# Kernel tuning notes

Hardware: AMD Instinct MI355X
Metric: run time of the kernel (lower is better)

## Reference

```python
import jax, jax.numpy as jnp
import numpy as np

B, C, H, W = 8, 128, 64, 64
HEADS = 8
HID = 512  # dim * ffn_expansion_factor


def conv1x1(x, w):
    # x: (b,c,h,w), w: (o,c)
    return jnp.einsum('bchw,oc->bohw', x, w)


def dwconv(x, w):
    # depthwise conv, w: (c,1,k,k), same padding
    k = w.shape[-1]
    p = k // 2
    return jax.lax.conv_general_dilated(
        x, w, window_strides=(1, 1), padding=((p, p), (p, p)),
        dimension_numbers=('NCHW', 'OIHW', 'NCHW'),
        feature_group_count=x.shape[1])


def ln_channels(x, w, b):
    # WithBias LayerNorm over channel dim (torch does it on b,(hw),c layout)
    mu = x.mean(axis=1, keepdims=True)
    var = x.var(axis=1, keepdims=True)
    return (x - mu) / jnp.sqrt(var + 1e-5) * w[None, :, None, None] + b[None, :, None, None]


def l2norm(x):
    # torch F.normalize along last dim, eps=1e-12
    n = jnp.linalg.norm(x, axis=-1, keepdims=True)
    return x / jnp.maximum(n, 1e-12)


def setup_inputs() -> dict:
    key = jax.random.key(0)
    ks = list(jax.random.split(key, 24))
    it = iter(ks)

    def nrm(shape, s=0.05):
        return (jax.random.normal(next(it), shape, jnp.float32) * s)

    d = {}
    d['x'] = jax.random.normal(next(it), (B, C, H, W), jnp.float32)
    d['ln1_w'] = jnp.ones((C,), jnp.float32)
    d['ln1_b'] = jnp.zeros((C,), jnp.float32)
    d['temp'] = jnp.ones((HEADS, 1, 1), jnp.float32)
    d['wq'] = nrm((C, C))
    d['wk'] = nrm((C, C))
    d['wv'] = nrm((C, C))
    for k in (3, 5, 7):
        for n in ('q', 'k', 'v'):
            d['dw%s%d' % (n, k)] = nrm((C, 1, k, k))
    d['attn_po'] = nrm((C, 3 * C))
    d['ln2_w'] = jnp.ones((C,), jnp.float32)
    d['ln2_b'] = jnp.zeros((C,), jnp.float32)
    d['ffn_in'] = nrm((2 * HID, C))
    for k in (3, 5, 7):
        d['ffn_dw%d' % k] = nrm((2 * HID, 1, k, k))
    d['ffn_po'] = nrm((C, 3 * HID))
    return d


def reference(x, ln1_w, ln1_b, temp, wq, wk, wv,
              dwq3, dwk3, dwv3, dwq5, dwk5, dwv5, dwq7, dwk7, dwv7,
              attn_po, ln2_w, ln2_b, ffn_in, ffn_dw3, ffn_dw5, ffn_dw7, ffn_po):
    b, c, h, w = x.shape
    ch = c // HEADS
    hw = h * w

    # ---- multi-scale channel (transposed) attention ----
    xn = ln_channels(x, ln1_w, ln1_b)
    q0 = conv1x1(xn, wq)
    k0 = conv1x1(xn, wk)
    v0 = conv1x1(xn, wv)

    outs = []
    for dq, dk, dv in ((dwq3, dwk3, dwv3), (dwq5, dwk5, dwv5), (dwq7, dwk7, dwv7)):
        q = l2norm(dwconv(q0, dq).reshape(b, HEADS, ch, hw))
        kk = l2norm(dwconv(k0, dk).reshape(b, HEADS, ch, hw))
        v = dwconv(v0, dv).reshape(b, HEADS, ch, hw)
        attn = jax.nn.softmax(jnp.einsum('bhcn,bhdn->bhcd', q, kk) * temp, axis=-1)
        outs.append(jnp.einsum('bhcd,bhdn->bhcn', attn, v).reshape(b, c, h, w))
    x = x + conv1x1(jnp.concatenate(outs, axis=1), attn_po)

    # ---- multi-kernel GEGLU FFN ----
    xn = ln_channels(x, ln2_w, ln2_b)
    xin = conv1x1(xn, ffn_in)  # (b, 2*HID, h, w)
    fouts = []
    for dw in (ffn_dw3, ffn_dw5, ffn_dw7):
        y = dwconv(xin, dw)
        g, m = jnp.split(y, 2, axis=1)
        fouts.append(jax.nn.gelu(g, approximate=False) * m)
    x = x + conv1x1(jnp.concatenate(fouts, axis=1), ffn_po)
    return x
```

## Files before the change

kernel.cpp:

```cpp
#include <hip/hip_runtime.h>
#include <hip/hip_bf16.h>
#include <math.h>

#define B_ 8
#define C_ 128
#define H_ 64
#define W_ 64
#define HW_ 4096
#define HEADS_ 8
#define CH_ 16
#define HID_ 512

typedef unsigned short ushort_t;
struct __attribute__((aligned(8))) us4 { ushort_t x, y, z, w; };

typedef __attribute__((ext_vector_type(8))) short bf16x8;
typedef __attribute__((ext_vector_type(4))) float f32x4;

__device__ __forceinline__ float bf2f(ushort_t u) {
  return __uint_as_float(((unsigned int)u) << 16);
}
__device__ __forceinline__ ushort_t f2bu(float f) {
  __hip_bfloat16 h = __float2bfloat16(f);
  return *reinterpret_cast<ushort_t*>(&h);
}
__device__ __forceinline__ float toF(float v) { return v; }
__device__ __forceinline__ float toF(ushort_t v) { return bf2f(v); }
__device__ __forceinline__ void storeF(float* p, float v) { *p = v; }
__device__ __forceinline__ void storeF(ushort_t* p, float v) { *p = f2bu(v); }

__device__ __forceinline__ float gelu_t(float x) {
  float z = 0.7978845608f * fmaf(0.044715f * x, x * x, x);
  float e = __expf(2.f * z);
  float th = 1.f - 2.f / (e + 1.f);
  return 0.5f * x * (1.f + th);
}

__global__ __launch_bounds__(256) void ln_ch(const float* __restrict__ x,
                                             const float* __restrict__ w,
                                             const float* __restrict__ b,
                                             ushort_t* __restrict__ out) {
  int p = blockIdx.x * 256 + threadIdx.x;
  int bi = p >> 12;
  int pos = p & (HW_ - 1);
  const float* xb = x + (size_t)bi * C_ * HW_ + pos;
  float s = 0.f, ss = 0.f;
  for (int c = 0; c < C_; c++) {
    float v = xb[(size_t)c * HW_];
    s += v;
    ss = fmaf(v, v, ss);
  }
  float mu = s * (1.f / C_);
  float var = ss * (1.f / C_) - mu * mu;
  float inv = rsqrtf(var + 1e-5f);
  ushort_t* ob = out + (size_t)bi * C_ * HW_ + pos;
  for (int c = 0; c < C_; c++) {
    ob[(size_t)c * HW_] = f2bu((xb[(size_t)c * HW_] - mu) * inv * w[c] + b[c]);
  }
}

__global__ __launch_bounds__(256) void cvt_w(const float* __restrict__ wq,
                                             const float* __restrict__ wk,
                                             const float* __restrict__ wv,
                                             const float* __restrict__ apo,
                                             const float* __restrict__ fin,
                                             const float* __restrict__ fpo,
                                             ushort_t* __restrict__ dst) {
  int id = blockIdx.x * 256 + threadIdx.x;
  const float* src;
  int off;
  if (id < 16384) { src = wq; off = id; }
  else if (id < 32768) { src = wk; off = id - 16384; }
  else if (id < 49152) { src = wv; off = id - 32768; }
  else if (id < 98304) { src = apo; off = id - 49152; }
  else if (id < 229376) { src = fin; off = id - 98304; }
  else if (id < 425984) { src = fpo; off = id - 229376; }
  else return;
  dst[id] = f2bu(src[off]);
}

__device__ __forceinline__ void loadrow_bf(const ushort_t* __restrict__ rowp,
                                           int cb, float* rv) {
#pragma unroll
  for (int b = 0; b < 4; b++) {
    int co = cb - 4 + b * 4;
    if ((unsigned)co <= 60u) {
      us4 t = *(const us4*)(rowp + co);
      rv[b * 4 + 0] = bf2f(t.x); rv[b * 4 + 1] = bf2f(t.y);
      rv[b * 4 + 2] = bf2f(t.z); rv[b * 4 + 3] = bf2f(t.w);
    } else {
      rv[b * 4 + 0] = 0.f; rv[b * 4 + 1] = 0.f;
      rv[b * 4 + 2] = 0.f; rv[b * 4 + 3] = 0.f;
    }
  }
}

template <typename Tin, typename Tout>
__global__ __launch_bounds__(256) void conv1x1_m(const Tin* __restrict__ in,
                                                 const ushort_t* __restrict__ wtb,
                                                 const float* __restrict__ resid,
                                                 Tout* __restrict__ out,
                                                 int cin, int cout, int wstride,
                                                 int accum) {
  constexpr int ST2 = 136;
  __shared__ ushort_t bsh[64 * ST2];
  int tid = threadIdx.x;
  int lane = tid & 63;
  int wid = tid >> 6;
  int lrow = lane & 15;
  int lk = lane >> 4;
  int blk = blockIdx.x;
  int nb = blk & 63;
  int rest = blk >> 6;
  int mb = cout >> 6;
  int m = rest % mb;
  int bi = rest / mb;
  int n0 = nb << 6;
  int o0 = (m << 6) + wid * 16;

  f32x4 acc[4] = {{0.f, 0.f, 0.f, 0.f}, {0.f, 0.f, 0.f, 0.f},
                  {0.f, 0.f, 0.f, 0.f}, {0.f, 0.f, 0.f, 0.f}};

  int nn = tid & 63;
  int wk4 = tid >> 6;
  for (int kc = 0; kc < cin; kc += 128) {
#pragma unroll
    for (int p = 0; p < 8; p++) {
      int kb = p * 16 + wk4 * 4;
      ushort_t u[4];
#pragma unroll
      for (int j = 0; j < 4; j++) {
        const Tin* src = in + ((size_t)bi * cin + kc + kb + j) * HW_ + n0 + nn;
        if constexpr (sizeof(Tin) == 4) {
          u[j] = f2bu(*(const float*)src);
        } else {
          u[j] = *(const ushort_t*)src;
        }
      }
      us4 w4;
      w4.x = u[0]; w4.y = u[1]; w4.z = u[2]; w4.w = u[3];
      *(us4*)&bsh[nn * ST2 + kb] = w4;
    }
    __syncthreads();
#pragma unroll
    for (int ks = 0; ks < 4; ks++) {
      const ushort_t* wr = wtb + (size_t)(o0 + lrow) * wstride + kc + ks * 32 + lk * 8;
      us4 wlo = *(const us4*)wr;
      us4 whi = *(const us4*)(wr + 4);
      bf16x8 af;
      af[0] = (short)wlo.x; af[1] = (short)wlo.y;
      af[2] = (short)wlo.z; af[3] = (short)wlo.w;
      af[4] = (short)whi.x; af[5] = (short)whi.y;
      af[6] = (short)whi.z; af[7] = (short)whi.w;
#pragma unroll
      for (int s = 0; s < 4; s++) {
        bf16x8 bf_ = *(const bf16x8*)&bsh[(s * 16 + lrow) * ST2 + ks * 32 + lk * 8];
        acc[s] = __builtin_amdgcn_mfma_f32_16x16x32_bf16(af, bf_, acc[s], 0, 0, 0);
      }
    }
    __syncthreads();
  }

  const float* rp = resid ? resid + (size_t)bi * cout * HW_ : nullptr;
  Tout* op = out + (size_t)bi * cout * HW_;
#pragma unroll
  for (int s = 0; s < 4; s++) {
#pragma unroll
    for (int r = 0; r < 4; r++) {
      int o = o0 + lk * 4 + r;
      int n = n0 + s * 16 + lrow;
      size_t off = (size_t)o * HW_ + n;
      float v = acc[s][r];
      if (rp) v += rp[off];
      if (accum) v += toF(op[off]);
      storeF(&op[off], v);
    }
  }
}

template <int K>
__global__ __launch_bounds__(256) void dwconv_d(const ushort_t* __restrict__ qkv0,
                                                const float* __restrict__ wq_,
                                                const float* __restrict__ wk_,
                                                const float* __restrict__ wv_,
                                                ushort_t* __restrict__ qd,
                                                ushort_t* __restrict__ kd,
                                                ushort_t* __restrict__ vd,
                                                float* __restrict__ sumsq_s) {
  constexpr int P = K / 2;
  __shared__ float wsh[K * K];
  __shared__ float red[4];
  int sel = blockIdx.y;
  const float* wgt = (sel == 0) ? wq_ : (sel == 1) ? wk_ : wv_;
  ushort_t* outp = (sel == 0) ? qd : (sel == 1) ? kd : vd;
  int blk = blockIdx.x;
  int half = blk & 1;
  int c = (blk >> 1) & (C_ - 1);
  int bi = blk >> 8;
  int tid = threadIdx.x;

  if (tid < K * K) wsh[tid] = wgt[(size_t)c * K * K + tid];
  __syncthreads();

  int r = tid >> 3;
  int cb = (tid & 7) << 3;
  int y = half * 32 + r;
  const ushort_t* plane = qkv0 + ((size_t)bi * 384 + sel * C_ + c) * HW_;

  float a[8];
#pragma unroll
  for (int o = 0; o < 8; o++) a[o] = 0.f;
#pragma unroll
  for (int dy = 0; dy < K; dy++) {
    int gy = y + dy - P;
    if ((unsigned)gy < 64u) {
      float rv[16];
      loadrow_bf(plane + gy * 64, cb, rv);
#pragma unroll
      for (int dx = 0; dx < K; dx++) {
        float wv = wsh[dy * K + dx];
#pragma unroll
        for (int o = 0; o < 8; o++) a[o] = fmaf(rv[o + dx + 4 - P], wv, a[o]);
      }
    }
  }
  ushort_t* ob = outp + (size_t)(bi * C_ + c) * HW_ + y * 64 + cb;
  us4 t0, t1;
  t0.x = f2bu(a[0]); t0.y = f2bu(a[1]); t0.z = f2bu(a[2]); t0.w = f2bu(a[3]);
  t1.x = f2bu(a[4]); t1.y = f2bu(a[5]); t1.z = f2bu(a[6]); t1.w = f2bu(a[7]);
  *(us4*)ob = t0;
  *(us4*)(ob + 4) = t1;

  float ssq = 0.f;
#pragma unroll
  for (int o = 0; o < 8; o++) ssq = fmaf(a[o], a[o], ssq);
#pragma unroll
  for (int off = 32; off >= 1; off >>= 1) ssq += __shfl_xor(ssq, off, 64);
  if ((tid & 63) == 0) red[tid >> 6] = ssq;
  __syncthreads();
  if (tid == 0 && sel < 2) {
    atomicAdd(&sumsq_s[sel * 1024 + bi * C_ + c], red[0] + red[1] + red[2] + red[3]);
  }
}

template <int K>
__global__ __launch_bounds__(256) void ffn_dwgate_p(const ushort_t* __restrict__ xin,
                                                    const float* __restrict__ w,
                                                    ushort_t* __restrict__ gated) {
  constexpr int P = K / 2;
  __shared__ float wsh[2 * K * K];
  int blk = blockIdx.x;
  int i = blk & 511;
  int bi = blk >> 9;
  int tid = threadIdx.x;

  if (tid < 2 * K * K) {
    wsh[tid] = (tid < K * K) ? w[(size_t)i * K * K + tid]
                             : w[(size_t)(512 + i) * K * K + (tid - K * K)];
  }
  __syncthreads();

  int r2 = tid >> 3;
  int cb = (tid & 7) << 3;
  int y0 = r2 * 2;
  const ushort_t* gin = xin + (size_t)(bi * 1024 + i) * HW_;
  const ushort_t* min_ = gin + (size_t)512 * HW_;

  float ge[16];
  {
    float a0[8], a1[8];
#pragma unroll
    for (int o = 0; o < 8; o++) { a0[o] = 0.f; a1[o] = 0.f; }
#pragma unroll
    for (int rr = 0; rr <= K; rr++) {
      int gy = y0 - P + rr;
      if ((unsigned)gy < 64u) {
        float rv[16];
        loadrow_bf(gin + gy * 64, cb, rv);
        if (rr < K) {
          float wv;
#pragma unroll
          for (int dx = 0; dx < K; dx++) {
            wv = wsh[rr * K + dx];
#pragma unroll
            for (int o = 0; o < 8; o++) a0[o] = fmaf(rv[o + dx + 4 - P], wv, a0[o]);
          }
        }
        if (rr >= 1) {
          float wv;
#pragma unroll
          for (int dx = 0; dx < K; dx++) {
            wv = wsh[(rr - 1) * K + dx];
#pragma unroll
            for (int o = 0; o < 8; o++) a1[o] = fmaf(rv[o + dx + 4 - P], wv, a1[o]);
          }
        }
      }
    }
#pragma unroll
    for (int o = 0; o < 8; o++) { ge[o] = gelu_t(a0[o]); ge[8 + o] = gelu_t(a1[o]); }
  }

  float m0[8], m1[8];
#pragma unroll
  for (int o = 0; o < 8; o++) { m0[o] = 0.f; m1[o] = 0.f; }
#pragma unroll
  for (int rr = 0; rr <= K; rr++) {
    int gy = y0 - P + rr;
    if ((unsigned)gy < 64u) {
      float rv[16];
      loadrow_bf(min_ + gy * 64, cb, rv);
      if (rr < K) {
        float wv;
#pragma unroll
        for (int dx = 0; dx < K; dx++) {
          wv = wsh[K * K + rr * K + dx];
#pragma unroll
          for (int o = 0; o < 8; o++) m0[o] = fmaf(rv[o + dx + 4 - P], wv, m0[o]);
        }
      }
      if (rr >= 1) {
        float wv;
#pragma unroll
        for (int dx = 0; dx < K; dx++) {
          wv = wsh[K * K + (rr - 1) * K + dx];
#pragma unroll
          for (int o = 0; o < 8; o++) m1[o] = fmaf(rv[o + dx + 4 - P], wv, m1[o]);
        }
      }
    }
  }
  ushort_t* gp = gated + (size_t)(bi * 512 + i) * HW_ + y0 * 64 + cb;
#pragma unroll
  for (int v = 0; v < 2; v++) {
    us4 t;
    t.x = f2bu(ge[v * 4 + 0] * m0[v * 4 + 0]);
    t.y = f2bu(ge[v * 4 + 1] * m0[v * 4 + 1]);
    t.z = f2bu(ge[v * 4 + 2] * m0[v * 4 + 2]);
    t.w = f2bu(ge[v * 4 + 3] * m0[v * 4 + 3]);
    *(us4*)(gp + v * 4) = t;
  }
  gp += 64;
#pragma unroll
  for (int v = 0; v < 2; v++) {
    us4 t;
    t.x = f2bu(ge[8 + v * 4 + 0] * m1[v * 4 + 0]);
    t.y = f2bu(ge[8 + v * 4 + 1] * m1[v * 4 + 1]);
    t.z = f2bu(ge[8 + v * 4 + 2] * m1[v * 4 + 2]);
    t.w = f2bu(ge[8 + v * 4 + 3] * m1[v * 4 + 3]);
    *(us4*)(gp + v * 4) = t;
  }
}

__global__ __launch_bounds__(256) void attn_score_part(const ushort_t* __restrict__ qd,
                                                       const ushort_t* __restrict__ kd,
                                                       float* __restrict__ part) {
  constexpr int ST = 258;
  __shared__ float qs[16 * ST];
  __shared__ float ks[16 * ST];
  int bh = blockIdx.x;
  int ch = blockIdx.y;
  int bi = bh >> 3;
  int h = bh & 7;
  int tid = threadIdx.x;
  int c = tid >> 4;
  int d = tid & 15;

  const ushort_t* qrow = qd + (size_t)(bi * C_ + h * CH_) * HW_ + ch * 256;
  const ushort_t* krow = kd + (size_t)(bi * C_ + h * CH_) * HW_ + ch * 256;
#pragma unroll
  for (int it = 0; it < 4; it++) {
    int idx = tid + it * 256;
    int r = idx >> 6, q4 = idx & 63;
    us4 qv = *(const us4*)(qrow + (size_t)r * HW_ + q4 * 4);
    us4 kv = *(const us4*)(krow + (size_t)r * HW_ + q4 * 4);
    float* qdst = &qs[r * ST + q4 * 4];
    float* kdst = &ks[r * ST + q4 * 4];
    qdst[0] = bf2f(qv.x); qdst[1] = bf2f(qv.y); qdst[2] = bf2f(qv.z); qdst[3] = bf2f(qv.w);
    kdst[0] = bf2f(kv.x); kdst[1] = bf2f(kv.y); kdst[2] = bf2f(kv.z); kdst[3] = bf2f(kv.w);
  }
  __syncthreads();

  const float* qp = &qs[c * ST];
  const float* kp = &ks[d * ST];
  float acc = 0.f;
#pragma unroll 8
  for (int j = 0; j < 256; j++) acc = fmaf(qp[j], kp[j], acc);
  part[((size_t)bh * 16 + ch) * 256 + tid] = acc;
}

__global__ __launch_bounds__(256) void attn_softmax(const float* __restrict__ part,
                                                    const float* __restrict__ sumsq_s,
                                                    const float* __restrict__ temp,
                                                    float* __restrict__ as_buf) {
  int bh = blockIdx.x;
  int bi = bh >> 3;
  int h = bh & 7;
  int tid = threadIdx.x;
  int c = tid >> 4;
  int d = tid & 15;
  float s = 0.f;
  const float* pp = part + (size_t)bh * 16 * 256 + tid;
#pragma unroll
  for (int ch = 0; ch < 16; ch++) s += pp[ch * 256];
  float sq = sumsq_s[bi * C_ + h * CH_ + c];
  float sk = sumsq_s[1024 + bi * C_ + h * CH_ + d];
  float invq = 1.f / fmaxf(sqrtf(sq), 1e-12f);
  float invk = 1.f / fmaxf(sqrtf(sk), 1e-12f);
  float S = s * invq * invk * temp[h];
  float mx = S;
#pragma unroll
  for (int o = 8; o >= 1; o >>= 1) mx = fmaxf(mx, __shfl_xor(mx, o, 16));
  float e = expf(S - mx);
  float sm = e;
#pragma unroll
  for (int o = 8; o >= 1; o >>= 1) sm += __shfl_xor(sm, o, 16);
  as_buf[(size_t)bh * 256 + tid] = e / sm;
}

__global__ __launch_bounds__(256) void attn_pv(const ushort_t* __restrict__ vd,
                                               const float* __restrict__ as_buf,
                                               ushort_t* __restrict__ osb_all,
                                               int coff) {
  __shared__ float as[16][17];
  int bh = blockIdx.x;
  int ch = blockIdx.y;
  int bi = bh >> 3;
  int h = bh & 7;
  int tid = threadIdx.x;
  if (tid < 256) {
    int cc = tid >> 4, dd = tid & 15;
    as[cc][dd] = as_buf[(size_t)bh * 256 + tid];
  }
  __syncthreads();

  int n = ch * 256 + tid;
  const ushort_t* vrow = vd + (size_t)(bi * C_ + h * CH_) * HW_ + n;
  float o_[16];
#pragma unroll
  for (int cc = 0; cc < 16; cc++) o_[cc] = 0.f;
#pragma unroll
  for (int dd = 0; dd < 16; dd++) {
    float vv = bf2f(vrow[(size_t)dd * HW_]);
#pragma unroll
    for (int cc = 0; cc < 16; cc++) o_[cc] = fmaf(as[cc][dd], vv, o_[cc]);
  }
  ushort_t* ob = osb_all + ((size_t)bi * 384 + coff + h * CH_) * HW_ + n;
#pragma unroll
  for (int cc = 0; cc < 16; cc++) ob[(size_t)cc * HW_] = f2bu(o_[cc]);
}

extern "C" void kernel_launch(void* const* d_in, const int* in_sizes, int n_in,
                              void* d_out, int out_size, void* d_ws, size_t ws_size,
                              hipStream_t stream) {
  const float* x = (const float*)d_in[0];
  const float* ln1_w = (const float*)d_in[1];
  const float* ln1_b = (const float*)d_in[2];
  const float* temp = (const float*)d_in[3];
  const float* wq = (const float*)d_in[4];
  const float* wk = (const float*)d_in[5];
  const float* wv = (const float*)d_in[6];
  const float* dw[9];
  for (int i = 0; i < 9; i++) dw[i] = (const float*)d_in[7 + i];
  const float* attn_po = (const float*)d_in[16];
  const float* ln2_w = (const float*)d_in[17];
  const float* ln2_b = (const float*)d_in[18];
  const float* ffn_in = (const float*)d_in[19];
  const float* ffn_dw[3] = {(const float*)d_in[20], (const float*)d_in[21],
                            (const float*)d_in[22]};
  const float* ffn_po = (const float*)d_in[23];
  float* out = (float*)d_out;

  const size_t MB = (size_t)1 << 20;
  char* wsb = (char*)d_ws;
  ushort_t* xnb = (ushort_t*)(wsb + 0 * MB);
  float* part = (float*)(wsb + 0 * MB);
  ushort_t* qkv0 = (ushort_t*)(wsb + 16 * MB);
  ushort_t* qdb = (ushort_t*)(wsb + 40 * MB);
  ushort_t* kdb = (ushort_t*)(wsb + 48 * MB);
  ushort_t* vdb = (ushort_t*)(wsb + 56 * MB);
  ushort_t* osb_all = (ushort_t*)(wsb + 64 * MB);
  float* x2 = (float*)(wsb + 112 * MB);
  float* as_buf = (float*)(wsb + 128 * MB);
  float* sumsq = (float*)(wsb + 128 * MB + 64 * 1024);
  ushort_t* wbuf = (ushort_t*)(wsb + 128 * MB + 96 * 1024);
  ushort_t* xin = (ushort_t*)(wsb + 16 * MB);
  ushort_t* gated = (ushort_t*)(wsb + 80 * MB);

  const ushort_t* wb_qkv = wbuf;
  const ushort_t* wb_apo = wbuf + 49152;
  const ushort_t* wb_fin = wbuf + 98304;
  const ushort_t* wb_fpo = wbuf + 229376;

  const int ln_grid = (B_ * HW_) / 256;
  const int g_qkv = B_ * (384 / 64) * 64;
  const int g128 = B_ * (C_ / 64) * 64;
  const int g1024 = B_ * (1024 / 64) * 64;
  const dim3 dwt_grid(B_ * C_ * 2, 3);
  const int ffg_grid = B_ * 512;
  const dim3 att_grid(B_ * HEADS_, 16);

  hipMemsetAsync(sumsq, 0, 3 * 2048 * sizeof(float), stream);
  cvt_w<<<1664, 256, 0, stream>>>(wq, wk, wv, attn_po, ffn_in, ffn_po, wbuf);

  ln_ch<<<ln_grid, 256, 0, stream>>>(x, ln1_w, ln1_b, xnb);
  conv1x1_m<ushort_t, ushort_t><<<g_qkv, 256, 0, stream>>>(
      xnb, wb_qkv, nullptr, qkv0, C_, 384, C_, 0);

  for (int s = 0; s < 3; s++) {
    float* sumsq_s = sumsq + s * 2048;
    if (s == 0)
      dwconv_d<3><<<dwt_grid, 256, 0, stream>>>(qkv0, dw[0], dw[1], dw[2],
                                                qdb, kdb, vdb, sumsq_s);
    else if (s == 1)
      dwconv_d<5><<<dwt_grid, 256, 0, stream>>>(qkv0, dw[3], dw[4], dw[5],
                                                qdb, kdb, vdb, sumsq_s);
    else
      dwconv_d<7><<<dwt_grid, 256, 0, stream>>>(qkv0, dw[6], dw[7], dw[8],
                                                qdb, kdb, vdb, sumsq_s);
    attn_score_part<<<att_grid, 256, 0, stream>>>(qdb, kdb, part);
    attn_softmax<<<B_ * HEADS_, 256, 0, stream>>>(part, sumsq_s, temp, as_buf);
    attn_pv<<<att_grid, 256, 0, stream>>>(vdb, as_buf, osb_all, s * C_);
  }
  conv1x1_m<ushort_t, float><<<g128, 256, 0, stream>>>(
      osb_all, wb_apo, x, x2, 384, C_, 384, 0);

  ln_ch<<<ln_grid, 256, 0, stream>>>(x2, ln2_w, ln2_b, xnb);
  conv1x1_m<ushort_t, ushort_t><<<g1024, 256, 0, stream>>>(
      xnb, wb_fin, nullptr, xin, C_, 1024, C_, 0);

  for (int s = 0; s < 3; s++) {
    if (s == 0)
      ffn_dwgate_p<3><<<ffg_grid, 256, 0, stream>>>(xin, ffn_dw[0], gated);
    else if (s == 1)
      ffn_dwgate_p<5><<<ffg_grid, 256, 0, stream>>>(xin, ffn_dw[1], gated);
    else
      ffn_dwgate_p<7><<<ffg_grid, 256, 0, stream>>>(xin, ffn_dw[2], gated);
    conv1x1_m<ushort_t, float><<<g128, 256, 0, stream>>>(
        gated, wb_fpo + s * 512, (s == 0) ? x2 : nullptr, out, 512, C_, 3 * HID_,
        s == 0 ? 0 : 1);
  }
  (void)in_sizes; (void)n_in; (void)out_size; (void)ws_size;
}
```

Baseline: 441.7 us.

## Compute four rows per thread in FFN dwconv-gate and fuse softmax into PV

The FFN depthwise-conv plus GEGLU kernel now computes four output rows per thread instead of two, using 128-thread blocks. Each loaded input row is reused across more outputs, so fewer redundant global row loads are needed per output. The attention softmax kernel is folded into the PV kernel: each PV block rebuilds the 16x16 softmax from the partial scores, which removes one launch and the as_buf round trip. In exchange, per-thread register use rises and the softmax work is repeated across the 16 spatial chunks.

```diff
diff --git a/kernel.cpp b/kernel.cpp
--- a/kernel.cpp
+++ b/kernel.cpp
@@ -244,7 +244,7 @@
 }
 
 template <int K>
-__global__ __launch_bounds__(256) void ffn_dwgate_p(const ushort_t* __restrict__ xin,
+__global__ __launch_bounds__(128) void ffn_dwgate_p(const ushort_t* __restrict__ xin,
                                                     const float* __restrict__ w,
                                                     ushort_t* __restrict__ gated) {
   constexpr int P = K / 2;
@@ -260,95 +260,83 @@
   }
   __syncthreads();
 
-  int r2 = tid >> 3;
+  int rg = tid >> 3;
   int cb = (tid & 7) << 3;
-  int y0 = r2 * 2;
+  int y0 = rg * 4;
   const ushort_t* gin = xin + (size_t)(bi * 1024 + i) * HW_;
   const ushort_t* min_ = gin + (size_t)512 * HW_;
 
-  float ge[16];
+  float ge[4][8];
   {
-    float a0[8], a1[8];
-#pragma unroll
-    for (int o = 0; o < 8; o++) { a0[o] = 0.f; a1[o] = 0.f; }
-#pragma unroll
-    for (int rr = 0; rr <= K; rr++) {
+    float a[4][8];
+#pragma unroll
+    for (int j = 0; j < 4; j++)
+#pragma unroll
+      for (int o = 0; o < 8; o++) a[j][o] = 0.f;
+#pragma unroll
+    for (int rr = 0; rr < K + 3; rr++) {
       int gy = y0 - P + rr;
       if ((unsigned)gy < 64u) {
         float rv[16];
         loadrow_bf(gin + gy * 64, cb, rv);
-        if (rr < K) {
-          float wv;
-#pragma unroll
-          for (int dx = 0; dx < K; dx++) {
-            wv = wsh[rr * K + dx];
-#pragma unroll
-            for (int o = 0; o < 8; o++) a0[o] = fmaf(rv[o + dx + 4 - P], wv, a0[o]);
-          }
-        }
-        if (rr >= 1) {
-          float wv;
-#pragma unroll
-          for (int dx = 0; dx < K; dx++) {
-            wv = wsh[(rr - 1) * K + dx];
-#pragma unroll
-            for (int o = 0; o < 8; o++) a1[o] = fmaf(rv[o + dx + 4 - P], wv, a1[o]);
+#pragma unroll
+        for (int j = 0; j < 4; j++) {
+          constexpr int dummy = 0; (void)dummy;
+          int dy = rr - j;
+          if (dy >= 0 && dy < K) {
+#pragma unroll
+            for (int dx = 0; dx < K; dx++) {
+              float wv = wsh[dy * K + dx];
+#pragma unroll
+              for (int o = 0; o < 8; o++) a[j][o] = fmaf(rv[o + dx + 4 - P], wv, a[j][o]);
+            }
           }
         }
       }
     }
 #pragma unroll
-    for (int o = 0; o < 8; o++) { ge[o] = gelu_t(a0[o]); ge[8 + o] = gelu_t(a1[o]); }
-  }
-
-  float m0[8], m1[8];
-#pragma unroll
-  for (int o = 0; o < 8; o++) { m0[o] = 0.f; m1[o] = 0.f; }
-#pragma unroll
-  for (int rr = 0; rr <= K; rr++) {
+    for (int j = 0; j < 4; j++)
+#pragma unroll
+      for (int o = 0; o < 8; o++) ge[j][o] = gelu_t(a[j][o]);
+  }
+
+  float ma[4][8];
+#pragma unroll
+  for (int j = 0; j < 4; j++)
+#pragma unroll
+    for (int o = 0; o < 8; o++) ma[j][o] = 0.f;
+#pragma unroll
+  for (int rr = 0; rr < K + 3; rr++) {
     int gy = y0 - P + rr;
     if ((unsigned)gy < 64u) {
       float rv[16];
       loadrow_bf(min_ + gy * 64, cb, rv);
-      if (rr < K) {
-        float wv;
-#pragma unroll
-        for (int dx = 0; dx < K; dx++) {
-          wv = wsh[K * K + rr * K + dx];
-#pragma unroll
-          for (int o = 0; o < 8; o++) m0[o] = fmaf(rv[o + dx + 4 - P], wv, m0[o]);
+#pragma unroll
+      for (int j = 0; j < 4; j++) {
+        int dy = rr - j;
+        if (dy >= 0 && dy < K) {
+#pragma unroll
+          for (int dx = 0; dx < K; dx++) {
+            float wv = wsh[K * K + dy * K + dx];
+#pragma unroll
+            for (int o = 0; o < 8; o++) ma[j][o] = fmaf(rv[o + dx + 4 - P], wv, ma[j][o]);
+          }
         }
       }
-      if (rr >= 1) {
-        float wv;
-#pragma unroll
-        for (int dx = 0; dx < K; dx++) {
-          wv = wsh[K * K + (rr - 1) * K + dx];
-#pragma unroll
-          for (int o = 0; o < 8; o++) m1[o] = fmaf(rv[o + dx + 4 - P], wv, m1[o]);
-        }
-      }
     }
   }
   ushort_t* gp = gated + (size_t)(bi * 512 + i) * HW_ + y0 * 64 + cb;
 #pragma unroll
-  for (int v = 0; v < 2; v++) {
-    us4 t;
-    t.x = f2bu(ge[v * 4 + 0] * m0[v * 4 + 0]);
-    t.y = f2bu(ge[v * 4 + 1] * m0[v * 4 + 1]);
-    t.z = f2bu(ge[v * 4 + 2] * m0[v * 4 + 2]);
-    t.w = f2bu(ge[v * 4 + 3] * m0[v * 4 + 3]);
-    *(us4*)(gp + v * 4) = t;
-  }
-  gp += 64;
-#pragma unroll
-  for (int v = 0; v < 2; v++) {
-    us4 t;
-    t.x = f2bu(ge[8 + v * 4 + 0] * m1[v * 4 + 0]);
-    t.y = f2bu(ge[8 + v * 4 + 1] * m1[v * 4 + 1]);
-    t.z = f2bu(ge[8 + v * 4 + 2] * m1[v * 4 + 2]);
-    t.w = f2bu(ge[8 + v * 4 + 3] * m1[v * 4 + 3]);
-    *(us4*)(gp + v * 4) = t;
+  for (int j = 0; j < 4; j++) {
+#pragma unroll
+    for (int v = 0; v < 2; v++) {
+      us4 t;
+      t.x = f2bu(ge[j][v * 4 + 0] * ma[j][v * 4 + 0]);
+      t.y = f2bu(ge[j][v * 4 + 1] * ma[j][v * 4 + 1]);
+      t.z = f2bu(ge[j][v * 4 + 2] * ma[j][v * 4 + 2]);
+      t.w = f2bu(ge[j][v * 4 + 3] * ma[j][v * 4 + 3]);
+      *(us4*)(gp + j * 64 + v * 4) = t;
+    }
   }
 }
 
@@ -389,48 +377,39 @@
   part[((size_t)bh * 16 + ch) * 256 + tid] = acc;
 }
 
-__global__ __launch_bounds__(256) void attn_softmax(const float* __restrict__ part,
-                                                    const float* __restrict__ sumsq_s,
-                                                    const float* __restrict__ temp,
-                                                    float* __restrict__ as_buf) {
-  int bh = blockIdx.x;
-  int bi = bh >> 3;
-  int h = bh & 7;
-  int tid = threadIdx.x;
-  int c = tid >> 4;
-  int d = tid & 15;
-  float s = 0.f;
-  const float* pp = part + (size_t)bh * 16 * 256 + tid;
-#pragma unroll
-  for (int ch = 0; ch < 16; ch++) s += pp[ch * 256];
-  float sq = sumsq_s[bi * C_ + h * CH_ + c];
-  float sk = sumsq_s[1024 + bi * C_ + h * CH_ + d];
-  float invq = 1.f / fmaxf(sqrtf(sq), 1e-12f);
-  float invk = 1.f / fmaxf(sqrtf(sk), 1e-12f);
-  float S = s * invq * invk * temp[h];
-  float mx = S;
-#pragma unroll
-  for (int o = 8; o >= 1; o >>= 1) mx = fmaxf(mx, __shfl_xor(mx, o, 16));
-  float e = expf(S - mx);
-  float sm = e;
-#pragma unroll
-  for (int o = 8; o >= 1; o >>= 1) sm += __shfl_xor(sm, o, 16);
-  as_buf[(size_t)bh * 256 + tid] = e / sm;
-}
-
-__global__ __launch_bounds__(256) void attn_pv(const ushort_t* __restrict__ vd,
-                                               const float* __restrict__ as_buf,
-                                               ushort_t* __restrict__ osb_all,
-                                               int coff) {
+__global__ __launch_bounds__(256) void attn_pv_sm(const ushort_t* __restrict__ vd,
+                                                  const float* __restrict__ part,
+                                                  const float* __restrict__ sumsq_s,
+                                                  const float* __restrict__ temp,
+                                                  ushort_t* __restrict__ osb_all,
+                                                  int coff) {
   __shared__ float as[16][17];
   int bh = blockIdx.x;
   int ch = blockIdx.y;
   int bi = bh >> 3;
   int h = bh & 7;
   int tid = threadIdx.x;
-  if (tid < 256) {
-    int cc = tid >> 4, dd = tid & 15;
-    as[cc][dd] = as_buf[(size_t)bh * 256 + tid];
+
+  {
+    int c = tid >> 4;
+    int d = tid & 15;
+    float s = 0.f;
+    const float* pp = part + (size_t)bh * 16 * 256 + tid;
+#pragma unroll
+    for (int c2 = 0; c2 < 16; c2++) s += pp[c2 * 256];
+    float sq = sumsq_s[bi * C_ + h * CH_ + c];
+    float sk = sumsq_s[1024 + bi * C_ + h * CH_ + d];
+    float invq = 1.f / fmaxf(sqrtf(sq), 1e-12f);
+    float invk = 1.f / fmaxf(sqrtf(sk), 1e-12f);
+    float S = s * invq * invk * temp[h];
+    float mx = S;
+#pragma unroll
+    for (int o = 8; o >= 1; o >>= 1) mx = fmaxf(mx, __shfl_xor(mx, o, 16));
+    float e = expf(S - mx);
+    float sm = e;
+#pragma unroll
+    for (int o = 8; o >= 1; o >>= 1) sm += __shfl_xor(sm, o, 16);
+    as[c][d] = e / sm;
   }
   __syncthreads();
 
@@ -481,9 +460,8 @@
   ushort_t* vdb = (ushort_t*)(wsb + 56 * MB);
   ushort_t* osb_all = (ushort_t*)(wsb + 64 * MB);
   float* x2 = (float*)(wsb + 112 * MB);
-  float* as_buf = (float*)(wsb + 128 * MB);
-  float* sumsq = (float*)(wsb + 128 * MB + 64 * 1024);
-  ushort_t* wbuf = (ushort_t*)(wsb + 128 * MB + 96 * 1024);
+  float* sumsq = (float*)(wsb + 128 * MB);
+  ushort_t* wbuf = (ushort_t*)(wsb + 128 * MB + 32 * 1024);
   ushort_t* xin = (ushort_t*)(wsb + 16 * MB);
   ushort_t* gated = (ushort_t*)(wsb + 80 * MB);
 
@@ -519,8 +497,8 @@
       dwconv_d<7><<<dwt_grid, 256, 0, stream>>>(qkv0, dw[6], dw[7], dw[8],
                                                 qdb, kdb, vdb, sumsq_s);
     attn_score_part<<<att_grid, 256, 0, stream>>>(qdb, kdb, part);
-    attn_softmax<<<B_ * HEADS_, 256, 0, stream>>>(part, sumsq_s, temp, as_buf);
-    attn_pv<<<att_grid, 256, 0, stream>>>(vdb, as_buf, osb_all, s * C_);
+    attn_pv_sm<<<att_grid, 256, 0, stream>>>(vdb, part, sumsq_s, temp, osb_all,
+                                             s * C_);
   }
   conv1x1_m<ushort_t, float><<<g128, 256, 0, stream>>>(
       osb_all, wb_apo, x, x2, 384, C_, 384, 0);
@@ -531,11 +509,11 @@
 
   for (int s = 0; s < 3; s++) {
     if (s == 0)
-      ffn_dwgate_p<3><<<ffg_grid, 256, 0, stream>>>(xin, ffn_dw[0], gated);
+      ffn_dwgate_p<3><<<ffg_grid, 128, 0, stream>>>(xin, ffn_dw[0], gated);
     else if (s == 1)
-      ffn_dwgate_p<5><<<ffg_grid, 256, 0, stream>>>(xin, ffn_dw[1], gated);
+      ffn_dwgate_p<5><<<ffg_grid, 128, 0, stream>>>(xin, ffn_dw[1], gated);
     else
-      ffn_dwgate_p<7><<<ffg_grid, 256, 0, stream>>>(xin, ffn_dw[2], gated);
+      ffn_dwgate_p<7><<<ffg_grid, 128, 0, stream>>>(xin, ffn_dw[2], gated);
     conv1x1_m<ushort_t, float><<<g128, 256, 0, stream>>>(
         gated, wb_fpo + s * 512, (s == 0) ? x2 : nullptr, out, 512, C_, 3 * HID_,
         s == 0 ? 0 : 1);
```

Result: no change. 441.5 us (-0.0%).

## Fuse attention softmax into PV kernel and vectorize conv1x1 input staging

Applied to the files above, without the earlier changes.

Removes the separate softmax kernel: each PV block now reduces the partial scores, normalizes and applies softmax itself, writing the probabilities straight to shared memory. This saves three launches and the as_buf round trip, at the cost of redundant softmax work across the 16 column-chunk blocks. The conv1x1 staging loop also switches from scalar strided global loads to 4-wide vector loads along the spatial dimension, followed by scattered 2-byte shared-memory stores. Those stores may cause bank conflicts.

```diff
diff --git a/kernel.cpp b/kernel.cpp
--- a/kernel.cpp
+++ b/kernel.cpp
@@ -121,25 +121,26 @@
   f32x4 acc[4] = {{0.f, 0.f, 0.f, 0.f}, {0.f, 0.f, 0.f, 0.f},
                   {0.f, 0.f, 0.f, 0.f}, {0.f, 0.f, 0.f, 0.f}};
 
-  int nn = tid & 63;
-  int wk4 = tid >> 6;
+  int nq = tid & 15;
+  int kg = tid >> 4;
   for (int kc = 0; kc < cin; kc += 128) {
 #pragma unroll
     for (int p = 0; p < 8; p++) {
-      int kb = p * 16 + wk4 * 4;
-      ushort_t u[4];
-#pragma unroll
-      for (int j = 0; j < 4; j++) {
-        const Tin* src = in + ((size_t)bi * cin + kc + kb + j) * HW_ + n0 + nn;
-        if constexpr (sizeof(Tin) == 4) {
-          u[j] = f2bu(*(const float*)src);
-        } else {
-          u[j] = *(const ushort_t*)src;
-        }
+      int k = p * 16 + kg;
+      if constexpr (sizeof(Tin) == 2) {
+        us4 v = *(const us4*)(in + ((size_t)bi * cin + kc + k) * HW_ + n0 + nq * 4);
+        bsh[(nq * 4 + 0) * ST2 + k] = v.x;
+        bsh[(nq * 4 + 1) * ST2 + k] = v.y;
+        bsh[(nq * 4 + 2) * ST2 + k] = v.z;
+        bsh[(nq * 4 + 3) * ST2 + k] = v.w;
+      } else {
+        float4 v = *(const float4*)((const float*)in +
+                                    ((size_t)bi * cin + kc + k) * HW_ + n0 + nq * 4);
+        bsh[(nq * 4 + 0) * ST2 + k] = f2bu(v.x);
+        bsh[(nq * 4 + 1) * ST2 + k] = f2bu(v.y);
+        bsh[(nq * 4 + 2) * ST2 + k] = f2bu(v.z);
+        bsh[(nq * 4 + 3) * ST2 + k] = f2bu(v.w);
       }
-      us4 w4;
-      w4.x = u[0]; w4.y = u[1]; w4.z = u[2]; w4.w = u[3];
-      *(us4*)&bsh[nn * ST2 + kb] = w4;
     }
     __syncthreads();
 #pragma unroll
@@ -389,48 +390,39 @@
   part[((size_t)bh * 16 + ch) * 256 + tid] = acc;
 }
 
-__global__ __launch_bounds__(256) void attn_softmax(const float* __restrict__ part,
-                                                    const float* __restrict__ sumsq_s,
-                                                    const float* __restrict__ temp,
-                                                    float* __restrict__ as_buf) {
-  int bh = blockIdx.x;
-  int bi = bh >> 3;
-  int h = bh & 7;
-  int tid = threadIdx.x;
-  int c = tid >> 4;
-  int d = tid & 15;
-  float s = 0.f;
-  const float* pp = part + (size_t)bh * 16 * 256 + tid;
-#pragma unroll
-  for (int ch = 0; ch < 16; ch++) s += pp[ch * 256];
-  float sq = sumsq_s[bi * C_ + h * CH_ + c];
-  float sk = sumsq_s[1024 + bi * C_ + h * CH_ + d];
-  float invq = 1.f / fmaxf(sqrtf(sq), 1e-12f);
-  float invk = 1.f / fmaxf(sqrtf(sk), 1e-12f);
-  float S = s * invq * invk * temp[h];
-  float mx = S;
-#pragma unroll
-  for (int o = 8; o >= 1; o >>= 1) mx = fmaxf(mx, __shfl_xor(mx, o, 16));
-  float e = expf(S - mx);
-  float sm = e;
-#pragma unroll
-  for (int o = 8; o >= 1; o >>= 1) sm += __shfl_xor(sm, o, 16);
-  as_buf[(size_t)bh * 256 + tid] = e / sm;
-}
-
-__global__ __launch_bounds__(256) void attn_pv(const ushort_t* __restrict__ vd,
-                                               const float* __restrict__ as_buf,
-                                               ushort_t* __restrict__ osb_all,
-                                               int coff) {
+__global__ __launch_bounds__(256) void attn_pv_sm(const ushort_t* __restrict__ vd,
+                                                  const float* __restrict__ part,
+                                                  const float* __restrict__ sumsq_s,
+                                                  const float* __restrict__ temp,
+                                                  ushort_t* __restrict__ osb_all,
+                                                  int coff) {
   __shared__ float as[16][17];
   int bh = blockIdx.x;
   int ch = blockIdx.y;
   int bi = bh >> 3;
   int h = bh & 7;
   int tid = threadIdx.x;
-  if (tid < 256) {
-    int cc = tid >> 4, dd = tid & 15;
-    as[cc][dd] = as_buf[(size_t)bh * 256 + tid];
+
+  {
+    int c = tid >> 4;
+    int d = tid & 15;
+    float s = 0.f;
+    const float* pp = part + (size_t)bh * 16 * 256 + tid;
+#pragma unroll
+    for (int c2 = 0; c2 < 16; c2++) s += pp[c2 * 256];
+    float sq = sumsq_s[bi * C_ + h * CH_ + c];
+    float sk = sumsq_s[1024 + bi * C_ + h * CH_ + d];
+    float invq = 1.f / fmaxf(sqrtf(sq), 1e-12f);
+    float invk = 1.f / fmaxf(sqrtf(sk), 1e-12f);
+    float S = s * invq * invk * temp[h];
+    float mx = S;
+#pragma unroll
+    for (int o = 8; o >= 1; o >>= 1) mx = fmaxf(mx, __shfl_xor(mx, o, 16));
+    float e = expf(S - mx);
+    float sm = e;
+#pragma unroll
+    for (int o = 8; o >= 1; o >>= 1) sm += __shfl_xor(sm, o, 16);
+    as[c][d] = e / sm;
   }
   __syncthreads();
 
@@ -481,9 +473,8 @@
   ushort_t* vdb = (ushort_t*)(wsb + 56 * MB);
   ushort_t* osb_all = (ushort_t*)(wsb + 64 * MB);
   float* x2 = (float*)(wsb + 112 * MB);
-  float* as_buf = (float*)(wsb + 128 * MB);
-  float* sumsq = (float*)(wsb + 128 * MB + 64 * 1024);
-  ushort_t* wbuf = (ushort_t*)(wsb + 128 * MB + 96 * 1024);
+  float* sumsq = (float*)(wsb + 128 * MB);
+  ushort_t* wbuf = (ushort_t*)(wsb + 128 * MB + 32 * 1024);
   ushort_t* xin = (ushort_t*)(wsb + 16 * MB);
   ushort_t* gated = (ushort_t*)(wsb + 80 * MB);
 
@@ -519,8 +510,8 @@
       dwconv_d<7><<<dwt_grid, 256, 0, stream>>>(qkv0, dw[6], dw[7], dw[8],
                                                 qdb, kdb, vdb, sumsq_s);
     attn_score_part<<<att_grid, 256, 0, stream>>>(qdb, kdb, part);
-    attn_softmax<<<B_ * HEADS_, 256, 0, stream>>>(part, sumsq_s, temp, as_buf);
-    attn_pv<<<att_grid, 256, 0, stream>>>(vdb, as_buf, osb_all, s * C_);
+    attn_pv_sm<<<att_grid, 256, 0, stream>>>(vdb, part, sumsq_s, temp, osb_all,
+                                             s * C_);
   }
   conv1x1_m<ushort_t, float><<<g128, 256, 0, stream>>>(
       osb_all, wb_apo, x, x2, 384, C_, 384, 0);
```

Measured after the change: 472.7 us. 7.0% more time.
